# Kernel tuning notes

Hardware: AMD Instinct MI355X
Metric: run time of the kernel (lower is better)

Reference implementation:

```python
import jax, jax.numpy as jnp
from jax import lax
import numpy as np

B, CIN, COUT, H, W = 8, 3, 16, 384, 384
WSCALE = 0.15  # keeps initial mean|x| < 3 so the while loop runs a few iterations


def conv1x1(x, w, b):
    # x: [B,C,H,W], w: [O,C], b: [O] -- 1x1 conv == channel-mixing GEMM
    return jnp.einsum('bchw,oc->bohw', x, w) + b[None, :, None, None]


def setup_inputs() -> dict:
    key = jax.random.key(0)
    ks = jax.random.split(key, 4)
    x = jax.random.normal(ks[0], (B, CIN, H, W), dtype=jnp.float32)
    w_pre = jax.random.normal(ks[1], (COUT, CIN), dtype=jnp.float32) * WSCALE
    b_pre = jnp.zeros((COUT,), dtype=jnp.float32)
    w_loop = jax.random.normal(ks[2], (COUT, COUT), dtype=jnp.float32) * WSCALE
    b_loop = jnp.zeros((COUT,), dtype=jnp.float32)
    w_shared = jax.random.normal(ks[3], (COUT, COUT), dtype=jnp.float32) * WSCALE
    b_shared = jnp.zeros((COUT,), dtype=jnp.float32)
    return {"x": x, "w_pre": w_pre, "b_pre": b_pre, "w_loop": w_loop,
            "b_loop": b_loop, "w_shared": w_shared, "b_shared": b_shared}


def reference(x, w_pre, b_pre, w_loop, b_loop, w_shared, b_shared):
    x = conv1x1(x, w_pre, b_pre)

    def cond_fn(v):
        return jnp.mean(jnp.abs(v)) < 3.0

    def body_fn(v):
        v = conv1x1(v, w_shared, b_shared)
        v = jnp.tanh(v)
        v = conv1x1(v, w_loop, b_loop)
        return v * 10.0

    x = lax.while_loop(cond_fn, body_fn, x)
    return conv1x1(x, w_shared, b_shared)
```

## Files before the change

### kernel.cpp

```cpp
#include <hip/hip_runtime.h>
#include <math.h>

#define BQ   8
#define CIN  3
#define COUT 16
#define HW   (384 * 384)
#define NPIX (BQ * HW)
#define NELT 18874368.0f
#define MAX_ITERS 16

#define TPB       256
#define NBLK      512
#define NTHREADS  (NBLK * TPB)
#define PPT       9

#define NLEAF        64
#define BLK_PER_LEAF (NBLK / NLEAF)

typedef float vfloat16 __attribute__((ext_vector_type(16)));

struct __align__(64) PadCnt { int cnt; int pad[15]; };

struct Ctl {
    PadCnt leaf[NLEAF];
    PadCnt root;
    PadCnt sense;
    float  partials[MAX_ITERS + 1][NBLK];
};

__global__ void k_init(Ctl* c) {
    int t = threadIdx.x;
    if (t < NLEAF) c->leaf[t].cnt = 0;
    if (t == 0) { c->root.cnt = 0; c->sense.cnt = 0; }
}

__device__ __forceinline__ float tanh_fast(float x) {
    float e = __expf(2.0f * x);
    return fmaf(-2.0f, __builtin_amdgcn_rcpf(e + 1.0f), 1.0f);
}

__device__ __forceinline__ float block_reduce_add(float v) {
    #pragma unroll
    for (int off = 32; off > 0; off >>= 1)
        v += __shfl_down(v, off, 64);
    __shared__ float red[TPB / 64];
    int lane = threadIdx.x & 63;
    int wid  = threadIdx.x >> 6;
    if (lane == 0) red[wid] = v;
    __syncthreads();
    float r = 0.f;
    if (threadIdx.x == 0) {
        #pragma unroll
        for (int i = 0; i < TPB / 64; ++i) r += red[i];
    }
    return r;
}

__device__ __forceinline__ void grid_barrier(Ctl* c, int* sense_sh) {
    __syncthreads();
    if (threadIdx.x == 0) {
        int next = *sense_sh ^ 1;
        int lf = blockIdx.x & (NLEAF - 1);
        int p = __hip_atomic_fetch_add(&c->leaf[lf].cnt, 1, __ATOMIC_ACQ_REL,
                                       __HIP_MEMORY_SCOPE_AGENT);
        if (p == BLK_PER_LEAF - 1) {
            __hip_atomic_store(&c->leaf[lf].cnt, 0, __ATOMIC_RELAXED,
                               __HIP_MEMORY_SCOPE_AGENT);
            int q = __hip_atomic_fetch_add(&c->root.cnt, 1, __ATOMIC_ACQ_REL,
                                           __HIP_MEMORY_SCOPE_AGENT);
            if (q == NLEAF - 1) {
                __hip_atomic_store(&c->root.cnt, 0, __ATOMIC_RELAXED,
                                   __HIP_MEMORY_SCOPE_AGENT);
                __hip_atomic_store(&c->sense.cnt, next, __ATOMIC_RELEASE,
                                   __HIP_MEMORY_SCOPE_AGENT);
            }
        }
        while (__hip_atomic_load(&c->sense.cnt, __ATOMIC_ACQUIRE,
                                 __HIP_MEMORY_SCOPE_AGENT) != next)
            __builtin_amdgcn_s_sleep(4);
        *sense_sh = next;
    }
    __syncthreads();
}

__device__ __forceinline__ float grid_sum(const float* part, float* bc) {
    int lane = threadIdx.x & 63, wid = threadIdx.x >> 6;
    if (wid == 0) {
        float s = 0.f;
        #pragma unroll
        for (int i = 0; i < NBLK / 64; ++i)
            s += __hip_atomic_load(&part[i * 64 + lane], __ATOMIC_RELAXED,
                                   __HIP_MEMORY_SCOPE_AGENT);
        #pragma unroll
        for (int off = 32; off > 0; off >>= 1)
            s += __shfl_down(s, off, 64);
        if (lane == 0) *bc = s;
    }
    __syncthreads();
    return *bc;
}


#define PRE_PIXEL(vk, kk)                                                \
    { int p = tid + (kk) * NTHREADS; int b = p / HW; int hw = p - b * HW;\
      const float* xb = x + (size_t)b * (CIN * HW) + hw;                 \
      float x0 = xb[0], x1 = xb[HW], x2 = xb[2 * HW];                    \
      _Pragma("unroll")                                                  \
      for (int o = 0; o < COUT; ++o) {                                   \
          float a = bp[o];                                               \
          a = fmaf(wp[o * CIN + 0], x0, a);                              \
          a = fmaf(wp[o * CIN + 1], x1, a);                              \
          a = fmaf(wp[o * CIN + 2], x2, a);                              \
          vk[o] = a; s += fabsf(a);                                      \
      } }

#define STEP_PIXEL(vk)                                                   \
    { float tt[COUT];                                                    \
      _Pragma("unroll")                                                  \
      for (int o = 0; o < COUT; ++o) {                                   \
          float a = bs[o];                                               \
          _Pragma("unroll")                                              \
          for (int c = 0; c < COUT; ++c)                                 \
              a = fmaf(ws[o * COUT + c], vk[c], a);                      \
          tt[o] = tanh_fast(a);                                          \
      }                                                                  \
      _Pragma("unroll")                                                  \
      for (int o = 0; o < COUT; ++o) {                                   \
          float a = bl[o];                                               \
          _Pragma("unroll")                                              \
          for (int c = 0; c < COUT; ++c)                                 \
              a = fmaf(wl[o * COUT + c], tt[c], a);                      \
          a *= 10.f;                                                     \
          vk[o] = a; s += fabsf(a);                                      \
      } }

#define FIN_PIXEL(vk, kk)                                                \
    { int p = tid + (kk) * NTHREADS; int b = p / HW; int hw = p - b * HW;\
      float* ob = out + (size_t)b * (COUT * HW) + hw;                    \
      _Pragma("unroll")                                                  \
      for (int o = 0; o < COUT; ++o) {                                   \
          float a = bs[o];                                               \
          _Pragma("unroll")                                              \
          for (int c = 0; c < COUT; ++c)                                 \
              a = fmaf(ws[o * COUT + c], vk[c], a);                      \
          ob[(size_t)o * HW] = a;                                        \
      } }

__global__ __launch_bounds__(TPB, 2) void k_persist(
        const float* __restrict__ x,
        const float* __restrict__ wp, const float* __restrict__ bp,
        const float* __restrict__ wl, const float* __restrict__ bl,
        const float* __restrict__ ws, const float* __restrict__ bs,
        float* __restrict__ out, Ctl* __restrict__ ctl) {
    __shared__ int sense_sh;
    __shared__ float bcast;
    const int t = threadIdx.x;
    if (t == 0) sense_sh = 0;
    __syncthreads();

    const int tid = blockIdx.x * TPB + t;

    vfloat16 v0, v1, v2, v3, v4, v5, v6, v7, v8;

    float s = 0.f;
    PRE_PIXEL(v0, 0) PRE_PIXEL(v1, 1) PRE_PIXEL(v2, 2)
    PRE_PIXEL(v3, 3) PRE_PIXEL(v4, 4) PRE_PIXEL(v5, 5)
    PRE_PIXEL(v6, 6) PRE_PIXEL(v7, 7) PRE_PIXEL(v8, 8)
    {
        float r = block_reduce_add(s);
        if (t == 0)
            __hip_atomic_store(&ctl->partials[0][blockIdx.x], r,
                               __ATOMIC_RELAXED, __HIP_MEMORY_SCOPE_AGENT);
    }
    grid_barrier(ctl, &sense_sh);

    int it = 0;
    while (it < MAX_ITERS) {
        float total = grid_sum(ctl->partials[it], &bcast);
        if (total >= 3.0f * NELT) break;

        s = 0.f;
        STEP_PIXEL(v0) STEP_PIXEL(v1) STEP_PIXEL(v2)
        STEP_PIXEL(v3) STEP_PIXEL(v4) STEP_PIXEL(v5)
        STEP_PIXEL(v6) STEP_PIXEL(v7) STEP_PIXEL(v8)
        ++it;
        float r = block_reduce_add(s);
        if (t == 0)
            __hip_atomic_store(&ctl->partials[it][blockIdx.x], r,
                               __ATOMIC_RELAXED, __HIP_MEMORY_SCOPE_AGENT);
        grid_barrier(ctl, &sense_sh);
    }

    FIN_PIXEL(v0, 0) FIN_PIXEL(v1, 1) FIN_PIXEL(v2, 2)
    FIN_PIXEL(v3, 3) FIN_PIXEL(v4, 4) FIN_PIXEL(v5, 5)
    FIN_PIXEL(v6, 6) FIN_PIXEL(v7, 7) FIN_PIXEL(v8, 8)
}

extern "C" void kernel_launch(void* const* d_in, const int* in_sizes, int n_in,
                              void* d_out, int out_size, void* d_ws, size_t ws_size,
                              hipStream_t stream) {
    const float* x  = (const float*)d_in[0];
    const float* wp = (const float*)d_in[1];
    const float* bp = (const float*)d_in[2];
    const float* wl = (const float*)d_in[3];
    const float* bl = (const float*)d_in[4];
    const float* ws = (const float*)d_in[5];
    const float* bs = (const float*)d_in[6];
    float* out = (float*)d_out;
    Ctl*   ctl = (Ctl*)d_ws;

    k_init<<<1, 64, 0, stream>>>(ctl);
    k_persist<<<NBLK, TPB, 0, stream>>>(x, wp, bp, wl, bl, ws, bs, out, ctl);
}
```

Before: 446.6 us.

## Run three blocks per CU with six pixels per thread, paired step

```diff
diff --git a/kernel.cpp b/kernel.cpp
--- a/kernel.cpp
+++ b/kernel.cpp
@@ -10,9 +10,10 @@
 #define MAX_ITERS 16
 
 #define TPB       256
-#define NBLK      512
+#define BPC       3
+#define NBLK      (BPC * 256)
 #define NTHREADS  (NBLK * TPB)
-#define PPT       9
+#define PPT       6
 
 #define NLEAF        64
 #define BLK_PER_LEAF (NBLK / NLEAF)
@@ -25,7 +26,7 @@
     PadCnt leaf[NLEAF];
     PadCnt root;
     PadCnt sense;
-    float  partials[MAX_ITERS + 1][NBLK];
+    float  partials[2][NBLK];
 };
 
 __global__ void k_init(Ctl* c) {
@@ -100,7 +101,6 @@
     return *bc;
 }
 
-
 #define PRE_PIXEL(vk, kk)                                                \
     { int p = tid + (kk) * NTHREADS; int b = p / HW; int hw = p - b * HW;\
       const float* xb = x + (size_t)b * (CIN * HW) + hw;                 \
@@ -114,24 +114,31 @@
           vk[o] = a; s += fabsf(a);                                      \
       } }
 
-#define STEP_PIXEL(vk)                                                   \
-    { float tt[COUT];                                                    \
-      _Pragma("unroll")                                                  \
-      for (int o = 0; o < COUT; ++o) {                                   \
-          float a = bs[o];                                               \
+#define STEP_PAIR(va, vb)                                                \
+    { float ua[COUT], ub[COUT];                                          \
+      _Pragma("unroll")                                                  \
+      for (int o = 0; o < COUT; ++o) {                                   \
+          float a0 = bs[o], a1 = bs[o];                                  \
           _Pragma("unroll")                                              \
-          for (int c = 0; c < COUT; ++c)                                 \
-              a = fmaf(ws[o * COUT + c], vk[c], a);                      \
-          tt[o] = tanh_fast(a);                                          \
+          for (int c = 0; c < COUT; ++c) {                               \
+              float w = ws[o * COUT + c];                                \
+              a0 = fmaf(w, va[c], a0);                                   \
+              a1 = fmaf(w, vb[c], a1);                                   \
+          }                                                              \
+          ua[o] = tanh_fast(a0); ub[o] = tanh_fast(a1);                  \
       }                                                                  \
       _Pragma("unroll")                                                  \
       for (int o = 0; o < COUT; ++o) {                                   \
-          float a = bl[o];                                               \
+          float a0 = bl[o], a1 = bl[o];                                  \
           _Pragma("unroll")                                              \
-          for (int c = 0; c < COUT; ++c)                                 \
-              a = fmaf(wl[o * COUT + c], tt[c], a);                      \
-          a *= 10.f;                                                     \
-          vk[o] = a; s += fabsf(a);                                      \
+          for (int c = 0; c < COUT; ++c) {                               \
+              float w = wl[o * COUT + c];                                \
+              a0 = fmaf(w, ua[c], a0);                                   \
+              a1 = fmaf(w, ub[c], a1);                                   \
+          }                                                              \
+          a0 *= 10.f; a1 *= 10.f;                                        \
+          va[o] = a0; vb[o] = a1;                                        \
+          s += fabsf(a0) + fabsf(a1);                                    \
       } }
 
 #define FIN_PIXEL(vk, kk)                                                \
@@ -146,7 +153,7 @@
           ob[(size_t)o * HW] = a;                                        \
       } }
 
-__global__ __launch_bounds__(TPB, 2) void k_persist(
+__global__ __launch_bounds__(TPB, BPC) void k_persist(
         const float* __restrict__ x,
         const float* __restrict__ wp, const float* __restrict__ bp,
         const float* __restrict__ wl, const float* __restrict__ bl,
@@ -160,12 +167,11 @@
 
     const int tid = blockIdx.x * TPB + t;
 
-    vfloat16 v0, v1, v2, v3, v4, v5, v6, v7, v8;
+    vfloat16 v0, v1, v2, v3, v4, v5;
 
     float s = 0.f;
     PRE_PIXEL(v0, 0) PRE_PIXEL(v1, 1) PRE_PIXEL(v2, 2)
     PRE_PIXEL(v3, 3) PRE_PIXEL(v4, 4) PRE_PIXEL(v5, 5)
-    PRE_PIXEL(v6, 6) PRE_PIXEL(v7, 7) PRE_PIXEL(v8, 8)
     {
         float r = block_reduce_add(s);
         if (t == 0)
@@ -176,24 +182,23 @@
 
     int it = 0;
     while (it < MAX_ITERS) {
-        float total = grid_sum(ctl->partials[it], &bcast);
+        float total = grid_sum(ctl->partials[it & 1], &bcast);
         if (total >= 3.0f * NELT) break;
 
         s = 0.f;
-        STEP_PIXEL(v0) STEP_PIXEL(v1) STEP_PIXEL(v2)
-        STEP_PIXEL(v3) STEP_PIXEL(v4) STEP_PIXEL(v5)
-        STEP_PIXEL(v6) STEP_PIXEL(v7) STEP_PIXEL(v8)
+        STEP_PAIR(v0, v1)
+        STEP_PAIR(v2, v3)
+        STEP_PAIR(v4, v5)
         ++it;
         float r = block_reduce_add(s);
         if (t == 0)
-            __hip_atomic_store(&ctl->partials[it][blockIdx.x], r,
+            __hip_atomic_store(&ctl->partials[it & 1][blockIdx.x], r,
                                __ATOMIC_RELAXED, __HIP_MEMORY_SCOPE_AGENT);
         grid_barrier(ctl, &sense_sh);
     }
 
     FIN_PIXEL(v0, 0) FIN_PIXEL(v1, 1) FIN_PIXEL(v2, 2)
     FIN_PIXEL(v3, 3) FIN_PIXEL(v4, 4) FIN_PIXEL(v5, 5)
-    FIN_PIXEL(v6, 6) FIN_PIXEL(v7, 7) FIN_PIXEL(v8, 8)
 }
 
 extern "C" void kernel_launch(void* const* d_in, const int* in_sizes, int n_in,
```

Measured after the change: 705.2 us. 57.9% more time.

## Fold grid reduction into barrier tree and broadcast stop flag

Applied to the files above, without the earlier changes.

```diff
diff --git a/kernel.cpp b/kernel.cpp
--- a/kernel.cpp
+++ b/kernel.cpp
@@ -10,33 +10,42 @@
 #define MAX_ITERS 16
 
 #define TPB       256
-#define NBLK      512
+#define BPC       2
+#define NBLK      (BPC * 256)
 #define NTHREADS  (NBLK * TPB)
 #define PPT       9
 
 #define NLEAF        64
 #define BLK_PER_LEAF (NBLK / NLEAF)
 
+#define SCOPE_AGENT __HIP_MEMORY_SCOPE_AGENT
+
 typedef float vfloat16 __attribute__((ext_vector_type(16)));
 
-struct __align__(64) PadCnt { int cnt; int pad[15]; };
+struct __align__(64) Node { int cnt; float acc; int pad[14]; };
 
 struct Ctl {
-    PadCnt leaf[NLEAF];
-    PadCnt root;
-    PadCnt sense;
-    float  partials[MAX_ITERS + 1][NBLK];
+    Node leaf[NLEAF];
+    Node root;
+    Node sense;
 };
 
 __global__ void k_init(Ctl* c) {
     int t = threadIdx.x;
-    if (t < NLEAF) c->leaf[t].cnt = 0;
-    if (t == 0) { c->root.cnt = 0; c->sense.cnt = 0; }
+    if (t < NLEAF) { c->leaf[t].cnt = 0; c->leaf[t].acc = 0.f; }
+    if (t == 0) {
+        c->root.cnt = 0; c->root.acc = 0.f;
+        c->sense.cnt = 0; c->sense.acc = 0.f;
+    }
 }
 
 __device__ __forceinline__ float tanh_fast(float x) {
     float e = __expf(2.0f * x);
     return fmaf(-2.0f, __builtin_amdgcn_rcpf(e + 1.0f), 1.0f);
+}
+
+__device__ __forceinline__ void vm_drain() {
+    asm volatile("s_waitcnt vmcnt(0)" ::: "memory");
 }
 
 __device__ __forceinline__ float block_reduce_add(float v) {
@@ -56,48 +65,53 @@
     return r;
 }
 
-__device__ __forceinline__ void grid_barrier(Ctl* c, int* sense_sh) {
-    __syncthreads();
+__device__ __forceinline__ int arrive_and_decide(Ctl* c, float v, int round,
+                                                 int* stop_sh) {
+    float r = block_reduce_add(v);
     if (threadIdx.x == 0) {
-        int next = *sense_sh ^ 1;
         int lf = blockIdx.x & (NLEAF - 1);
-        int p = __hip_atomic_fetch_add(&c->leaf[lf].cnt, 1, __ATOMIC_ACQ_REL,
-                                       __HIP_MEMORY_SCOPE_AGENT);
+        __hip_atomic_fetch_add(&c->leaf[lf].acc, r, __ATOMIC_RELAXED, SCOPE_AGENT);
+        vm_drain();
+        int p = __hip_atomic_fetch_add(&c->leaf[lf].cnt, 1, __ATOMIC_RELAXED,
+                                       SCOPE_AGENT);
         if (p == BLK_PER_LEAF - 1) {
-            __hip_atomic_store(&c->leaf[lf].cnt, 0, __ATOMIC_RELAXED,
-                               __HIP_MEMORY_SCOPE_AGENT);
-            int q = __hip_atomic_fetch_add(&c->root.cnt, 1, __ATOMIC_ACQ_REL,
-                                           __HIP_MEMORY_SCOPE_AGENT);
+            float sl = __hip_atomic_exchange(&c->leaf[lf].acc, 0.0f,
+                                             __ATOMIC_RELAXED, SCOPE_AGENT);
+            __hip_atomic_exchange(&c->leaf[lf].cnt, 0, __ATOMIC_RELAXED,
+                                  SCOPE_AGENT);
+            vm_drain();
+            __hip_atomic_fetch_add(&c->root.acc, sl, __ATOMIC_RELAXED,
+                                   SCOPE_AGENT);
+            vm_drain();
+            int q = __hip_atomic_fetch_add(&c->root.cnt, 1, __ATOMIC_RELAXED,
+                                           SCOPE_AGENT);
             if (q == NLEAF - 1) {
-                __hip_atomic_store(&c->root.cnt, 0, __ATOMIC_RELAXED,
-                                   __HIP_MEMORY_SCOPE_AGENT);
-                __hip_atomic_store(&c->sense.cnt, next, __ATOMIC_RELEASE,
-                                   __HIP_MEMORY_SCOPE_AGENT);
+                float total = __hip_atomic_exchange(&c->root.acc, 0.0f,
+                                                    __ATOMIC_RELAXED, SCOPE_AGENT);
+                __hip_atomic_exchange(&c->root.cnt, 0, __ATOMIC_RELAXED,
+                                      SCOPE_AGENT);
+                vm_drain();
+                int stop = (total >= 3.0f * NELT) ? 1 : 0;
+                __hip_atomic_exchange(&c->sense.cnt, (round << 1) | stop,
+                                      __ATOMIC_RELAXED, SCOPE_AGENT);
             }
         }
-        while (__hip_atomic_load(&c->sense.cnt, __ATOMIC_ACQUIRE,
-                                 __HIP_MEMORY_SCOPE_AGENT) != next)
-            __builtin_amdgcn_s_sleep(4);
-        *sense_sh = next;
+        int s, polls = 0;
+        for (;;) {
+            if ((polls & 7) == 0)
+                s = __hip_atomic_fetch_add(&c->sense.cnt, 0, __ATOMIC_RELAXED,
+                                           SCOPE_AGENT);
+            else
+                s = __hip_atomic_load(&c->sense.cnt, __ATOMIC_RELAXED,
+                                      SCOPE_AGENT);
+            if ((s >> 1) >= round) break;
+            ++polls;
+            __builtin_amdgcn_s_sleep(8);
+        }
+        *stop_sh = s & 1;
     }
     __syncthreads();
-}
-
-__device__ __forceinline__ float grid_sum(const float* part, float* bc) {
-    int lane = threadIdx.x & 63, wid = threadIdx.x >> 6;
-    if (wid == 0) {
-        float s = 0.f;
-        #pragma unroll
-        for (int i = 0; i < NBLK / 64; ++i)
-            s += __hip_atomic_load(&part[i * 64 + lane], __ATOMIC_RELAXED,
-                                   __HIP_MEMORY_SCOPE_AGENT);
-        #pragma unroll
-        for (int off = 32; off > 0; off >>= 1)
-            s += __shfl_down(s, off, 64);
-        if (lane == 0) *bc = s;
-    }
-    __syncthreads();
-    return *bc;
+    return *stop_sh;
 }
 
 
@@ -146,18 +160,14 @@
           ob[(size_t)o * HW] = a;                                        \
       } }
 
-__global__ __launch_bounds__(TPB, 2) void k_persist(
+__global__ __launch_bounds__(TPB, BPC) void k_persist(
         const float* __restrict__ x,
         const float* __restrict__ wp, const float* __restrict__ bp,
         const float* __restrict__ wl, const float* __restrict__ bl,
         const float* __restrict__ ws, const float* __restrict__ bs,
         float* __restrict__ out, Ctl* __restrict__ ctl) {
-    __shared__ int sense_sh;
-    __shared__ float bcast;
+    __shared__ int stop_sh;
     const int t = threadIdx.x;
-    if (t == 0) sense_sh = 0;
-    __syncthreads();
-
     const int tid = blockIdx.x * TPB + t;
 
     vfloat16 v0, v1, v2, v3, v4, v5, v6, v7, v8;
@@ -166,29 +176,18 @@
     PRE_PIXEL(v0, 0) PRE_PIXEL(v1, 1) PRE_PIXEL(v2, 2)
     PRE_PIXEL(v3, 3) PRE_PIXEL(v4, 4) PRE_PIXEL(v5, 5)
     PRE_PIXEL(v6, 6) PRE_PIXEL(v7, 7) PRE_PIXEL(v8, 8)
-    {
-        float r = block_reduce_add(s);
-        if (t == 0)
-            __hip_atomic_store(&ctl->partials[0][blockIdx.x], r,
-                               __ATOMIC_RELAXED, __HIP_MEMORY_SCOPE_AGENT);
-    }
-    grid_barrier(ctl, &sense_sh);
+
+    int round = 1;
+    int stop = arrive_and_decide(ctl, s, round, &stop_sh);
 
     int it = 0;
-    while (it < MAX_ITERS) {
-        float total = grid_sum(ctl->partials[it], &bcast);
-        if (total >= 3.0f * NELT) break;
-
+    while (!stop && it < MAX_ITERS) {
         s = 0.f;
         STEP_PIXEL(v0) STEP_PIXEL(v1) STEP_PIXEL(v2)
         STEP_PIXEL(v3) STEP_PIXEL(v4) STEP_PIXEL(v5)
         STEP_PIXEL(v6) STEP_PIXEL(v7) STEP_PIXEL(v8)
-        ++it;
-        float r = block_reduce_add(s);
-        if (t == 0)
-            __hip_atomic_store(&ctl->partials[it][blockIdx.x], r,
-                               __ATOMIC_RELAXED, __HIP_MEMORY_SCOPE_AGENT);
-        grid_barrier(ctl, &sense_sh);
+        ++it; ++round;
+        stop = arrive_and_decide(ctl, s, round, &stop_sh);
     }
 
     FIN_PIXEL(v0, 0) FIN_PIXEL(v1, 1) FIN_PIXEL(v2, 2)
```

Measured after the change: 514.7 us. +15.2%, slower.
